# Performance work log

Hardware: AMD Instinct MI355X
Metric: run time of the kernel (lower is better)

Reference implementation:

```python
import jax, jax.numpy as jnp
import numpy as np

CUBE_SIZE = 24
N_NEURONS = CUBE_SIZE ** 3  # 13824
INPUT_DIM = 512
OUTPUT_DIM = 1000
MAX_STEPS = 30
BATCH = 256


def _build_neighbor_indices(size: int) -> np.ndarray:
    """[N, 27] int32; invalid (out-of-cube) neighbors map to pad slot N."""
    n = size ** 3
    c = np.arange(size)
    z, y, x = np.meshgrid(c, c, c, indexing='ij')  # each [size,size,size]
    cols = []
    for dz in (-1, 0, 1):
        for dy in (-1, 0, 1):
            for dx in (-1, 0, 1):
                nz, ny, nx = z + dz, y + dy, x + dx
                valid = ((nz >= 0) & (nz < size) & (ny >= 0) & (ny < size)
                         & (nx >= 0) & (nx < size))
                idx = nz * size * size + ny * size + nx
                cols.append(np.where(valid, idx, n))
    return np.stack(cols, axis=-1).reshape(n, 27).astype(np.int32)


def setup_inputs() -> dict:
    key = jax.random.key(0)
    ks = jax.random.split(key, 4)
    # xavier-ish small init scales (gain 0.5 style)
    w_in = jax.random.normal(ks[0], (N_NEURONS, INPUT_DIM), jnp.float32) * 0.01
    w_local = jax.random.normal(ks[1], (N_NEURONS, 27), jnp.float32) * 0.1
    w_out = jax.random.normal(ks[2], (OUTPUT_DIM, N_NEURONS), jnp.float32) * 0.01
    x = jax.random.normal(ks[3], (BATCH, INPUT_DIM), jnp.float32)
    return {
        'x': x,
        'W_in_w': w_in,
        'W_in_b': jnp.zeros((N_NEURONS,), jnp.float32),
        'W_local': w_local,
        'W_out_w': w_out,
        'W_out_b': jnp.zeros((OUTPUT_DIM,), jnp.float32),
        'neighbor_indices': jnp.asarray(_build_neighbor_indices(CUBE_SIZE)),
    }


def reference(x, W_in_w, W_in_b, W_local, W_out_w, W_out_b, neighbor_indices):
    batch = x.shape[0]
    x_proj = x @ W_in_w.T + W_in_b  # [B, N]
    h0 = jnp.zeros((batch, N_NEURONS), x.dtype)
    pad = jnp.zeros((batch, 1), x.dtype)

    def step(h, _):
        h_padded = jnp.concatenate([h, pad], axis=1)        # [B, N+1]
        nbr = h_padded[:, neighbor_indices]                  # [B, N, 27]
        weighted = jnp.einsum('bnk,nk->bn', nbr, W_local)    # [B, N]
        return jnp.tanh(x_proj + weighted), None

    h, _ = jax.lax.scan(step, h0, None, length=MAX_STEPS)
    return h @ W_out_w.T + W_out_b  # [B, output_dim]
```

## Files before the change

### kernel.cpp

```cpp
#include <hip/hip_runtime.h>
#include <hip/hip_bf16.h>

#define NN   13824
#define BB   256
#define KDIM 512
#define ODIM 1000
#define CUBE 24
#define KS   16

typedef short bf8 __attribute__((ext_vector_type(8)));
typedef float f32x4 __attribute__((ext_vector_type(4)));

__device__ __forceinline__ float fast_tanh(float a) {
    float e = __expf(2.0f * a);
    return 1.0f - 2.0f / (e + 1.0f);
}
__device__ __forceinline__ float bf_lo(unsigned u) { return __uint_as_float(u << 16); }
__device__ __forceinline__ float bf_hi(unsigned u) { return __uint_as_float(u & 0xffff0000u); }
__device__ __forceinline__ unsigned short bf_rne(float f) {
    unsigned u = __float_as_uint(f);
    u += 0x7fffu + ((u >> 16) & 1u);
    return (unsigned short)(u >> 16);
}
__device__ __forceinline__ unsigned pk_bf16(float lo, float hi) {
    union { __hip_bfloat162 h; unsigned u; } cv;
    cv.h = __float22bfloat162_rn(make_float2(lo, hi));
    return cv.u;
}
__device__ __forceinline__ bf8 cvt8(float4 a, float4 b) {
    union { bf8 v; unsigned u[4]; } r;
    r.u[0] = pk_bf16(a.x, a.y);
    r.u[1] = pk_bf16(a.z, a.w);
    r.u[2] = pk_bf16(b.x, b.y);
    r.u[3] = pk_bf16(b.z, b.w);
    return r.v;
}

__global__ __launch_bounds__(256) void xbf_kernel(
    const float* __restrict__ x, unsigned* __restrict__ xb)
{
    int i = blockIdx.x * 256 + threadIdx.x;
    float2 v = *(const float2*)&x[(size_t)i * 2];
    xb[i] = pk_bf16(v.x, v.y);
}

__global__ __launch_bounds__(256) void xproj_mfma(
    const float* __restrict__ w_in, const float* __restrict__ bias,
    const short* __restrict__ xbf, unsigned short* __restrict__ xp,
    unsigned short* __restrict__ h1)
{
    const int tid = threadIdx.x, w = tid >> 6, lane = tid & 63;
    const int quad = lane >> 4, l16 = lane & 15;
    const int n0 = blockIdx.x * 16;
    const float* __restrict__ arow = &w_in[(size_t)(n0 + l16) * KDIM];

    f32x4 acc[4] = {};

    int ka = quad * 8;
    float4 a0 = *(const float4*)&arow[ka];
    float4 a1 = *(const float4*)&arow[ka + 4];
    bf8 bb[4];
#pragma unroll
    for (int j = 0; j < 4; ++j)
        bb[j] = *(const bf8*)&xbf[(size_t)(w * 64 + j * 16 + l16) * KDIM + ka];

    for (int it = 0; it < 16; ++it) {
        float4 na0{}, na1{}; bf8 nb[4] = {};
        if (it < 15) {
            const int nka = ka + 32;
            na0 = *(const float4*)&arow[nka];
            na1 = *(const float4*)&arow[nka + 4];
#pragma unroll
            for (int j = 0; j < 4; ++j)
                nb[j] = *(const bf8*)&xbf[(size_t)(w * 64 + j * 16 + l16) * KDIM + nka];
        }
        bf8 af = cvt8(a0, a1);
#pragma unroll
        for (int j = 0; j < 4; ++j)
            acc[j] = __builtin_amdgcn_mfma_f32_16x16x32_bf16(af, bb[j], acc[j], 0, 0, 0);
        a0 = na0; a1 = na1;
#pragma unroll
        for (int j = 0; j < 4; ++j) bb[j] = nb[j];
        ka += 32;
    }

#pragma unroll
    for (int j = 0; j < 4; ++j) {
        const int b = w * 64 + j * 16 + l16;
#pragma unroll
        for (int r = 0; r < 4; ++r) {
            const int n = n0 + quad * 4 + r;
            const float v = acc[j][r] + bias[n];
            xp[(size_t)n * BB + b] = bf_rne(v);
            h1[(size_t)n * BB + b] = bf_rne(fast_tanh(v));
        }
    }
}

__device__ __forceinline__ void load_plane_f2(
    const unsigned* __restrict__ h32, int z, int y, int xx, int dof, float2* w9)
{
#pragma unroll
    for (int j = 0; j < 9; ++j) {
        const int dz = j / 3 - 1, dy = j % 3 - 1;
        const int zz = z + dz, yy = y + dy;
        const bool valid = (xx >= 0) & (xx < CUBE) & (zz >= 0) & (zz < CUBE) &
                           (yy >= 0) & (yy < CUBE);
        unsigned v = 0u;
        if (valid) v = h32[(size_t)((zz * 24 + yy) * 24 + xx) * 128 + dof];
        w9[j] = make_float2(bf_lo(v), bf_hi(v));
    }
}

__global__ __launch_bounds__(128) void step_kernel(
    const unsigned* __restrict__ hprev, const unsigned* __restrict__ xp,
    const float* __restrict__ wl, unsigned* __restrict__ hnext)
{
    const int tid  = threadIdx.x;
    const int wv   = __builtin_amdgcn_readfirstlane(tid >> 6);
    const int lane = tid & 63;

    const int bid   = blockIdx.x;
    const int zhi   = bid & 7;
    const int inner = bid >> 3;
    const int y     = inner % 24;
    const int r     = inner / 24;
    const int xc    = r & 3;
    const int zlo   = r >> 2;
    const int z     = zhi * 3 + zlo;

    const int x0   = xc * 6;
    const int dof  = wv * 64 + lane;

    float2 win[5][9];
    load_plane_f2(hprev, z, y, x0 - 1, dof, win[0]);
    load_plane_f2(hprev, z, y, x0,     dof, win[1]);
    load_plane_f2(hprev, z, y, x0 + 1, dof, win[2]);
    load_plane_f2(hprev, z, y, x0 + 2, dof, win[3]);

#pragma unroll
    for (int xi = 0; xi < 6; ++xi) {
        const int x = x0 + xi;
        if (xi <= 3)
            load_plane_f2(hprev, z, y, x + 3, dof, win[(xi + 4) % 5]);

        const int n = (z * 24 + y) * 24 + x;
        const float* __restrict__ wn = &wl[(size_t)n * 27];
        const unsigned xpv = xp[(size_t)n * 128 + dof];
        float2 acc = make_float2(bf_lo(xpv), bf_hi(xpv));

        const float2* pm = win[xi % 5];
        const float2* pc = win[(xi + 1) % 5];
        const float2* pp = win[(xi + 2) % 5];
#pragma unroll
        for (int j = 0; j < 9; ++j) {
            const float w0 = wn[3 * j + 0];
            const float w1 = wn[3 * j + 1];
            const float w2 = wn[3 * j + 2];
            acc.x += w0 * pm[j].x + w1 * pc[j].x + w2 * pp[j].x;
            acc.y += w0 * pm[j].y + w1 * pc[j].y + w2 * pp[j].y;
        }
        hnext[(size_t)n * 128 + dof] = pk_bf16(fast_tanh(acc.x), fast_tanh(acc.y));
    }
}

__global__ __launch_bounds__(256) void transpose_kernel(
    const unsigned* __restrict__ h32, unsigned* __restrict__ hT32)
{
    __shared__ unsigned short T[64][66];
    const int tid = threadIdx.x;
    const int rr = tid >> 2, g = tid & 3;
    const int k0 = blockIdx.x * 64, b0 = blockIdx.y * 64;
#pragma unroll
    for (int i = 0; i < 8; ++i) {
        unsigned d = h32[(size_t)(k0 + rr) * 128 + b0 / 2 + g * 8 + i];
        const int bl = (g * 8 + i) * 2;
        T[bl][rr]     = (unsigned short)(d & 0xffffu);
        T[bl + 1][rr] = (unsigned short)(d >> 16);
    }
    __syncthreads();
#pragma unroll
    for (int i = 0; i < 8; ++i) {
        const int kl = (g * 8 + i) * 2;
        unsigned d = (unsigned)T[rr][kl] | ((unsigned)T[rr][kl + 1] << 16);
        hT32[(size_t)(b0 + rr) * (NN / 2) + k0 / 2 + g * 8 + i] = d;
    }
}

__global__ __launch_bounds__(256) void outgemm_mfma(
    const float* __restrict__ wout, const short* __restrict__ hT,
    float* __restrict__ part)
{
    const int tid = threadIdx.x, w = tid >> 6, lane = tid & 63;
    const int quad = lane >> 4, l16 = lane & 15;
    const int o0 = blockIdx.x * 32;
    const int kb = blockIdx.y * (NN / KS);
    const int b0 = w * 64;

    const int oa = o0 + l16, ob = o0 + 16 + l16;
    const bool av0 = oa < ODIM, av1 = ob < ODIM;
    const float* __restrict__ ar0 = &wout[(size_t)oa * NN];
    const float* __restrict__ ar1 = &wout[(size_t)ob * NN];
    const float4 z4 = {0.f, 0.f, 0.f, 0.f};

    f32x4 acc[2][4] = {};

    int ka = kb + quad * 8;
    float4 a00 = av0 ? *(const float4*)&ar0[ka]     : z4;
    float4 a01 = av0 ? *(const float4*)&ar0[ka + 4] : z4;
    float4 a10 = av1 ? *(const float4*)&ar1[ka]     : z4;
    float4 a11 = av1 ? *(const float4*)&ar1[ka + 4] : z4;
    bf8 bb[4];
#pragma unroll
    for (int j = 0; j < 4; ++j)
        bb[j] = *(const bf8*)&hT[(size_t)(b0 + j * 16 + l16) * NN + ka];

    for (int it = 0; it < 27; ++it) {
        float4 na00{}, na01{}, na10{}, na11{}; bf8 nb[4] = {};
        if (it < 26) {
            const int nka = ka + 32;
            na00 = av0 ? *(const float4*)&ar0[nka]     : z4;
            na01 = av0 ? *(const float4*)&ar0[nka + 4] : z4;
            na10 = av1 ? *(const float4*)&ar1[nka]     : z4;
            na11 = av1 ? *(const float4*)&ar1[nka + 4] : z4;
#pragma unroll
            for (int j = 0; j < 4; ++j)
                nb[j] = *(const bf8*)&hT[(size_t)(b0 + j * 16 + l16) * NN + nka];
        }
        bf8 af0 = cvt8(a00, a01);
        bf8 af1 = cvt8(a10, a11);
#pragma unroll
        for (int j = 0; j < 4; ++j) {
            acc[0][j] = __builtin_amdgcn_mfma_f32_16x16x32_bf16(af0, bb[j], acc[0][j], 0, 0, 0);
            acc[1][j] = __builtin_amdgcn_mfma_f32_16x16x32_bf16(af1, bb[j], acc[1][j], 0, 0, 0);
        }
        a00 = na00; a01 = na01; a10 = na10; a11 = na11;
#pragma unroll
        for (int j = 0; j < 4; ++j) bb[j] = nb[j];
        ka += 32;
    }

#pragma unroll
    for (int i = 0; i < 2; ++i)
#pragma unroll
        for (int j = 0; j < 4; ++j) {
            const int b = b0 + j * 16 + l16;
#pragma unroll
            for (int r = 0; r < 4; ++r) {
                const int o = o0 + i * 16 + quad * 4 + r;
                part[((size_t)blockIdx.y * 1024 + o) * BB + b] = acc[i][j][r];
            }
        }
}

__global__ __launch_bounds__(256) void reduce_kernel(
    const float* __restrict__ part, const float* __restrict__ bias,
    float* __restrict__ out)
{
    const int o = blockIdx.x, b = threadIdx.x;
    float s = bias[o];
#pragma unroll
    for (int kc = 0; kc < KS; ++kc)
        s += part[((size_t)kc * 1024 + o) * BB + b];
    out[(size_t)b * ODIM + o] = s;
}

extern "C" void kernel_launch(void* const* d_in, const int* in_sizes, int n_in,
                              void* d_out, int out_size, void* d_ws, size_t ws_size,
                              hipStream_t stream)
{
    const float* x       = (const float*)d_in[0];
    const float* w_in    = (const float*)d_in[1];
    const float* b_in    = (const float*)d_in[2];
    const float* w_local = (const float*)d_in[3];
    const float* w_out   = (const float*)d_in[4];
    const float* b_out   = (const float*)d_in[5];
    float* out = (float*)d_out;

    char* p = (char*)d_ws;
    unsigned short* xp_bf = (unsigned short*)p;          p += (size_t)NN * BB * 2;
    unsigned short* hA    = (unsigned short*)p;          p += (size_t)NN * BB * 2;
    unsigned short* hB    = (unsigned short*)p;          p += (size_t)NN * BB * 2;
    unsigned short* hT    = (unsigned short*)p;          p += (size_t)NN * BB * 2;
    unsigned short* x_bf  = (unsigned short*)p;          p += (size_t)BB * KDIM * 2;
    float*          part  = (float*)p;

    xbf_kernel<<<256, 256, 0, stream>>>(x, (unsigned*)x_bf);
    xproj_mfma<<<864, 256, 0, stream>>>(w_in, b_in, (const short*)x_bf, xp_bf, hA);

    const unsigned* hp = (const unsigned*)hA;
    unsigned* hn = (unsigned*)hB;
    for (int s = 0; s < 29; ++s) {
        step_kernel<<<2304, 128, 0, stream>>>(hp, (const unsigned*)xp_bf, w_local, hn);
        unsigned* t = (unsigned*)hp; hp = hn; hn = t;
    }

    transpose_kernel<<<dim3(216, 4), 256, 0, stream>>>(hp, (unsigned*)hT);
    outgemm_mfma<<<dim3(32, KS), 256, 0, stream>>>(w_out, (const short*)hT, part);
    reduce_kernel<<<ODIM, 256, 0, stream>>>(part, b_out, out);
}
```

Before: 573.4 us.

## Run all recurrent steps in one LDS-resident cube kernel per batch pair

Replaces the 29 per-step launches with one persistent kernel. Each workgroup keeps a padded 26^3 fp16 cube for two batch columns in shared memory, double-buffered, and iterates every step with packed fp16 dot2 stencils, which removes the global-memory round trips and launch overhead between steps. The local weights are pre-packed to fp16 and the output GEMM switches to fp16 MFMA, with the split-K factor reduced. This relies on about 140KB of dynamic LDS per workgroup and uses only 128 workgroups, and fp16 lowers precision for the stencil weights and activations.

```diff
diff --git a/kernel.cpp b/kernel.cpp
--- a/kernel.cpp
+++ b/kernel.cpp
@@ -6,9 +6,18 @@
 #define KDIM 512
 #define ODIM 1000
 #define CUBE 24
-#define KS   16
+#define KS   12
+
+#define PC    26
+#define PLANE (PC*PC)
+#define PCUBE (PC*PC*PC)
+#define COLU  17576
+#define BUFU  35152
+#define LDSB  140608
 
 typedef short bf8 __attribute__((ext_vector_type(8)));
+typedef _Float16 h8 __attribute__((ext_vector_type(8)));
+typedef _Float16 h2 __attribute__((ext_vector_type(2)));
 typedef float f32x4 __attribute__((ext_vector_type(4)));
 
 __device__ __forceinline__ float fast_tanh(float a) {
@@ -29,10 +38,32 @@
 }
 __device__ __forceinline__ bf8 cvt8(float4 a, float4 b) {
     union { bf8 v; unsigned u[4]; } r;
-    r.u[0] = pk_bf16(a.x, a.y);
-    r.u[1] = pk_bf16(a.z, a.w);
-    r.u[2] = pk_bf16(b.x, b.y);
-    r.u[3] = pk_bf16(b.z, b.w);
+    r.u[0] = pk_bf16(a.x, a.y); r.u[1] = pk_bf16(a.z, a.w);
+    r.u[2] = pk_bf16(b.x, b.y); r.u[3] = pk_bf16(b.z, b.w);
+    return r.v;
+}
+__device__ __forceinline__ unsigned short f16b(float a) {
+    union { _Float16 h; unsigned short s; } c; c.h = (_Float16)a; return c.s;
+}
+__device__ __forceinline__ h2 u2h(unsigned u) {
+    union { unsigned u; h2 h; } c; c.u = u; return c.h;
+}
+__device__ __forceinline__ float f16lo(unsigned u) { return (float)u2h(u).x; }
+__device__ __forceinline__ float f16hi(unsigned u) { return (float)u2h(u).y; }
+#if __has_builtin(__builtin_amdgcn_fdot2)
+__device__ __forceinline__ float dot2(unsigned w, unsigned v, float acc) {
+    return __builtin_amdgcn_fdot2(u2h(w), u2h(v), acc, false);
+}
+#else
+__device__ __forceinline__ float dot2(unsigned w, unsigned v, float acc) {
+    h2 W = u2h(w), V = u2h(v);
+    return acc + (float)W.x * (float)V.x + (float)W.y * (float)V.y;
+}
+#endif
+__device__ __forceinline__ h8 cvt8f(float4 a, float4 b) {
+    union { h8 v; unsigned short s[8]; } r;
+    r.s[0] = f16b(a.x); r.s[1] = f16b(a.y); r.s[2] = f16b(a.z); r.s[3] = f16b(a.w);
+    r.s[4] = f16b(b.x); r.s[5] = f16b(b.y); r.s[6] = f16b(b.z); r.s[7] = f16b(b.w);
     return r.v;
 }
 
@@ -44,10 +75,25 @@
     xb[i] = pk_bf16(v.x, v.y);
 }
 
+__global__ __launch_bounds__(256) void wprep_kernel(
+    const float* __restrict__ wl, unsigned* __restrict__ wab,
+    unsigned short* __restrict__ wc)
+{
+    int n = blockIdx.x * 256 + threadIdx.x;
+#pragma unroll
+    for (int j = 0; j < 9; ++j) {
+        float w0 = wl[n * 27 + 3 * j + 0];
+        float w1 = wl[n * 27 + 3 * j + 1];
+        float w2 = wl[n * 27 + 3 * j + 2];
+        wab[j * NN + n] = (unsigned)f16b(w0) | ((unsigned)f16b(w1) << 16);
+        wc[j * NN + n]  = f16b(w2);
+    }
+}
+
 __global__ __launch_bounds__(256) void xproj_mfma(
     const float* __restrict__ w_in, const float* __restrict__ bias,
-    const short* __restrict__ xbf, unsigned short* __restrict__ xp,
-    unsigned short* __restrict__ h1)
+    const short* __restrict__ xbf, unsigned short* __restrict__ xpT_u,
+    unsigned short* __restrict__ xp_bf, unsigned short* __restrict__ h1)
 {
     const int tid = threadIdx.x, w = tid >> 6, lane = tid & 63;
     const int quad = lane >> 4, l16 = lane & 15;
@@ -91,9 +137,97 @@
         for (int r = 0; r < 4; ++r) {
             const int n = n0 + quad * 4 + r;
             const float v = acc[j][r] + bias[n];
-            xp[(size_t)n * BB + b] = bf_rne(v);
-            h1[(size_t)n * BB + b] = bf_rne(fast_tanh(v));
-        }
+            xp_bf[(size_t)n * BB + b] = bf_rne(v);
+            h1[(size_t)n * BB + b]    = bf_rne(fast_tanh(v));
+            xpT_u[((size_t)(b >> 1) * NN + n) * 2 + (b & 1)] = f16b(v);
+        }
+    }
+}
+
+__global__ __launch_bounds__(512) void cube_kernel(
+    const unsigned* __restrict__ xpT,
+    const unsigned* __restrict__ wab,
+    const unsigned short* __restrict__ wc,
+    unsigned short* __restrict__ hT)
+{
+    extern __shared__ char smem[];
+    unsigned*        sdw = (unsigned*)smem;
+    unsigned short*  sus = (unsigned short*)smem;
+    const int tid = threadIdx.x;
+    const int cp  = blockIdx.x;
+
+    for (int i = tid; i < (LDSB / 4); i += 512) sdw[i] = 0u;
+    __syncthreads();
+
+#pragma unroll 1
+    for (int k = 0; k < 14; ++k) {
+        int p = tid + k * 512;
+        if (p >= 6912) break;
+        int line = p / 12, xq = p - line * 12, x0 = 2 * xq;
+        int z = line / 24, y = line - z * 24;
+        int n0 = line * 24 + x0;
+        uint2 xq2 = *(const uint2*)&xpT[(size_t)cp * NN + n0];
+        int Pi = ((z + 1) * PC + (y + 1)) * PC + x0 + 1;
+        sus[Pi]            = f16b(fast_tanh(f16lo(xq2.x)));
+        sus[Pi + 1]        = f16b(fast_tanh(f16lo(xq2.y)));
+        sus[COLU + Pi]     = f16b(fast_tanh(f16hi(xq2.x)));
+        sus[COLU + Pi + 1] = f16b(fast_tanh(f16hi(xq2.y)));
+    }
+    __syncthreads();
+
+    int cur = 0;
+#pragma unroll 1
+    for (int s = 0; s < 29; ++s) {
+        const int curU = cur * BUFU;
+        const int nxtU = curU ^ BUFU;
+#pragma unroll 1
+        for (int k = 0; k < 14; ++k) {
+            int p = tid + k * 512;
+            if (p >= 6912) break;
+            int line = p / 12, xq = p - line * 12, x0 = 2 * xq;
+            int z = line / 24, y = line - z * 24;
+            int n0 = line * 24 + x0;
+            int pb = curU + (z * PC + y) * PC + x0;
+
+            uint2 xq2 = *(const uint2*)&xpT[(size_t)cp * NN + n0];
+            float a00 = f16lo(xq2.x), a01 = f16hi(xq2.x);
+            float a10 = f16lo(xq2.y), a11 = f16hi(xq2.y);
+#pragma unroll
+            for (int j = 0; j < 9; ++j) {
+                const int off = (j / 3) * PLANE + (j % 3) * PC;
+                unsigned d0c0 = *(const unsigned*)&sus[pb + off];
+                unsigned d1c0 = *(const unsigned*)&sus[pb + off + 2];
+                unsigned d0c1 = *(const unsigned*)&sus[pb + off + COLU];
+                unsigned d1c1 = *(const unsigned*)&sus[pb + off + COLU + 2];
+                uint2 w2v = *(const uint2*)&wab[(size_t)j * NN + n0];
+                unsigned wcd = *(const unsigned*)&wc[(size_t)j * NN + n0];
+                unsigned wB0 = wcd & 0xffffu;
+                unsigned wB1 = wcd >> 16;
+                a00 = dot2(w2v.x, d0c0, a00); a00 = dot2(wB0, d1c0, a00);
+                a01 = dot2(w2v.x, d0c1, a01); a01 = dot2(wB0, d1c1, a01);
+                unsigned s1c0 = __builtin_amdgcn_alignbit(d1c0, d0c0, 16);
+                unsigned s3c0 = d1c0 >> 16;
+                unsigned s1c1 = __builtin_amdgcn_alignbit(d1c1, d0c1, 16);
+                unsigned s3c1 = d1c1 >> 16;
+                a10 = dot2(w2v.y, s1c0, a10); a10 = dot2(wB1, s3c0, a10);
+                a11 = dot2(w2v.y, s1c1, a11); a11 = dot2(wB1, s3c1, a11);
+            }
+            int Pw = nxtU + (pb - curU) + PLANE + PC + 1;
+            sus[Pw]            = f16b(fast_tanh(a00));
+            sus[Pw + 1]        = f16b(fast_tanh(a10));
+            sus[Pw + COLU]     = f16b(fast_tanh(a01));
+            sus[Pw + COLU + 1] = f16b(fast_tanh(a11));
+        }
+        __syncthreads();
+        cur ^= 1;
+    }
+
+    const int fU = cur * BUFU;
+    for (int n = tid; n < NN; n += 512) {
+        int z = n / 576, r = n - z * 576, y = r / 24, x = r - y * 24;
+        int P = fU + ((z + 1) * PC + (y + 1)) * PC + x + 1;
+        hT[(size_t)(2 * cp) * NN + n]     = sus[P];
+        hT[(size_t)(2 * cp + 1) * NN + n] = sus[P + COLU];
     }
 }
 
@@ -119,7 +253,6 @@
     const int tid  = threadIdx.x;
     const int wv   = __builtin_amdgcn_readfirstlane(tid >> 6);
     const int lane = tid & 63;
-
     const int bid   = blockIdx.x;
     const int zhi   = bid & 7;
     const int inner = bid >> 3;
@@ -128,9 +261,8 @@
     const int xc    = r & 3;
     const int zlo   = r >> 2;
     const int z     = zhi * 3 + zlo;
-
-    const int x0   = xc * 6;
-    const int dof  = wv * 64 + lane;
+    const int x0    = xc * 6;
+    const int dof   = wv * 64 + lane;
 
     float2 win[5][9];
     load_plane_f2(hprev, z, y, x0 - 1, dof, win[0]);
@@ -141,22 +273,17 @@
 #pragma unroll
     for (int xi = 0; xi < 6; ++xi) {
         const int x = x0 + xi;
-        if (xi <= 3)
-            load_plane_f2(hprev, z, y, x + 3, dof, win[(xi + 4) % 5]);
-
+        if (xi <= 3) load_plane_f2(hprev, z, y, x + 3, dof, win[(xi + 4) % 5]);
         const int n = (z * 24 + y) * 24 + x;
         const float* __restrict__ wn = &wl[(size_t)n * 27];
         const unsigned xpv = xp[(size_t)n * 128 + dof];
         float2 acc = make_float2(bf_lo(xpv), bf_hi(xpv));
-
         const float2* pm = win[xi % 5];
         const float2* pc = win[(xi + 1) % 5];
         const float2* pp = win[(xi + 2) % 5];
 #pragma unroll
         for (int j = 0; j < 9; ++j) {
-            const float w0 = wn[3 * j + 0];
-            const float w1 = wn[3 * j + 1];
-            const float w2 = wn[3 * j + 2];
+            const float w0 = wn[3 * j], w1 = wn[3 * j + 1], w2 = wn[3 * j + 2];
             acc.x += w0 * pm[j].x + w1 * pc[j].x + w2 * pp[j].x;
             acc.y += w0 * pm[j].y + w1 * pc[j].y + w2 * pp[j].y;
         }
@@ -164,7 +291,7 @@
     }
 }
 
-__global__ __launch_bounds__(256) void transpose_kernel(
+__global__ __launch_bounds__(256) void transpose_cvt(
     const unsigned* __restrict__ h32, unsigned* __restrict__ hT32)
 {
     __shared__ unsigned short T[64][66];
@@ -182,13 +309,15 @@
 #pragma unroll
     for (int i = 0; i < 8; ++i) {
         const int kl = (g * 8 + i) * 2;
-        unsigned d = (unsigned)T[rr][kl] | ((unsigned)T[rr][kl + 1] << 16);
-        hT32[(size_t)(b0 + rr) * (NN / 2) + k0 / 2 + g * 8 + i] = d;
+        float fa = __uint_as_float((unsigned)T[rr][kl] << 16);
+        float fb = __uint_as_float((unsigned)T[rr][kl + 1] << 16);
+        hT32[(size_t)(b0 + rr) * (NN / 2) + k0 / 2 + g * 8 + i] =
+            (unsigned)f16b(fa) | ((unsigned)f16b(fb) << 16);
     }
 }
 
 __global__ __launch_bounds__(256) void outgemm_mfma(
-    const float* __restrict__ wout, const short* __restrict__ hT,
+    const float* __restrict__ wout, const _Float16* __restrict__ hT,
     float* __restrict__ part)
 {
     const int tid = threadIdx.x, w = tid >> 6, lane = tid & 63;
@@ -210,14 +339,15 @@
     float4 a01 = av0 ? *(const float4*)&ar0[ka + 4] : z4;
     float4 a10 = av1 ? *(const float4*)&ar1[ka]     : z4;
     float4 a11 = av1 ? *(const float4*)&ar1[ka + 4] : z4;
-    bf8 bb[4];
+    h8 bb[4];
 #pragma unroll
     for (int j = 0; j < 4; ++j)
-        bb[j] = *(const bf8*)&hT[(size_t)(b0 + j * 16 + l16) * NN + ka];
-
-    for (int it = 0; it < 27; ++it) {
-        float4 na00{}, na01{}, na10{}, na11{}; bf8 nb[4] = {};
-        if (it < 26) {
+        bb[j] = *(const h8*)&hT[(size_t)(b0 + j * 16 + l16) * NN + ka];
+
+    const int ITER = (NN / KS) / 32;
+    for (int it = 0; it < ITER; ++it) {
+        float4 na00{}, na01{}, na10{}, na11{}; h8 nb[4] = {};
+        if (it < ITER - 1) {
             const int nka = ka + 32;
             na00 = av0 ? *(const float4*)&ar0[nka]     : z4;
             na01 = av0 ? *(const float4*)&ar0[nka + 4] : z4;
@@ -225,14 +355,14 @@
             na11 = av1 ? *(const float4*)&ar1[nka + 4] : z4;
 #pragma unroll
             for (int j = 0; j < 4; ++j)
-                nb[j] = *(const bf8*)&hT[(size_t)(b0 + j * 16 + l16) * NN + nka];
-        }
-        bf8 af0 = cvt8(a00, a01);
-        bf8 af1 = cvt8(a10, a11);
+                nb[j] = *(const h8*)&hT[(size_t)(b0 + j * 16 + l16) * NN + nka];
+        }
+        h8 af0 = cvt8f(a00, a01);
+        h8 af1 = cvt8f(a10, a11);
 #pragma unroll
         for (int j = 0; j < 4; ++j) {
-            acc[0][j] = __builtin_amdgcn_mfma_f32_16x16x32_bf16(af0, bb[j], acc[0][j], 0, 0, 0);
-            acc[1][j] = __builtin_amdgcn_mfma_f32_16x16x32_bf16(af1, bb[j], acc[1][j], 0, 0, 0);
+            acc[0][j] = __builtin_amdgcn_mfma_f32_16x16x32_f16(af0, bb[j], acc[0][j], 0, 0, 0);
+            acc[1][j] = __builtin_amdgcn_mfma_f32_16x16x32_f16(af1, bb[j], acc[1][j], 0, 0, 0);
         }
         a00 = na00; a01 = na01; a10 = na10; a11 = na11;
 #pragma unroll
@@ -278,24 +408,36 @@
     float* out = (float*)d_out;
 
     char* p = (char*)d_ws;
-    unsigned short* xp_bf = (unsigned short*)p;          p += (size_t)NN * BB * 2;
-    unsigned short* hA    = (unsigned short*)p;          p += (size_t)NN * BB * 2;
-    unsigned short* hB    = (unsigned short*)p;          p += (size_t)NN * BB * 2;
-    unsigned short* hT    = (unsigned short*)p;          p += (size_t)NN * BB * 2;
-    unsigned short* x_bf  = (unsigned short*)p;          p += (size_t)BB * KDIM * 2;
-    float*          part  = (float*)p;
+    unsigned*       xpT   = (unsigned*)p;        p += (size_t)128 * NN * 4;
+    unsigned short* hT    = (unsigned short*)p;  p += (size_t)256 * NN * 2;
+    unsigned short* x_bf  = (unsigned short*)p;  p += (size_t)BB * KDIM * 2;
+    unsigned*       wab   = (unsigned*)p;        p += (size_t)9 * NN * 4;
+    unsigned short* wc    = (unsigned short*)p;  p += (size_t)9 * NN * 2;
+    unsigned short* xp_bf = (unsigned short*)p;  p += (size_t)NN * BB * 2;
+    unsigned short* hA    = (unsigned short*)p;  p += (size_t)NN * BB * 2;
+    unsigned short* hB    = (unsigned short*)p;  p += (size_t)NN * BB * 2;
+    float* part = (float*)xp_bf;
 
     xbf_kernel<<<256, 256, 0, stream>>>(x, (unsigned*)x_bf);
-    xproj_mfma<<<864, 256, 0, stream>>>(w_in, b_in, (const short*)x_bf, xp_bf, hA);
-
-    const unsigned* hp = (const unsigned*)hA;
-    unsigned* hn = (unsigned*)hB;
-    for (int s = 0; s < 29; ++s) {
-        step_kernel<<<2304, 128, 0, stream>>>(hp, (const unsigned*)xp_bf, w_local, hn);
-        unsigned* t = (unsigned*)hp; hp = hn; hn = t;
-    }
-
-    transpose_kernel<<<dim3(216, 4), 256, 0, stream>>>(hp, (unsigned*)hT);
-    outgemm_mfma<<<dim3(32, KS), 256, 0, stream>>>(w_out, (const short*)hT, part);
+    wprep_kernel<<<54, 256, 0, stream>>>(w_local, wab, wc);
+    xproj_mfma<<<864, 256, 0, stream>>>(w_in, b_in, (const short*)x_bf,
+                                        (unsigned short*)xpT, xp_bf, hA);
+
+    bool fast = hipFuncSetAttribute((const void*)cube_kernel,
+        hipFuncAttributeMaxDynamicSharedMemorySize, LDSB) == hipSuccess;
+
+    if (fast) {
+        cube_kernel<<<128, 512, LDSB, stream>>>(xpT, wab, wc, hT);
+    } else {
+        const unsigned* hp = (const unsigned*)hA;
+        unsigned* hn = (unsigned*)hB;
+        for (int s = 0; s < 29; ++s) {
+            step_kernel<<<2304, 128, 0, stream>>>(hp, (const unsigned*)xp_bf, w_local, hn);
+            unsigned* t = (unsigned*)hp; hp = hn; hn = t;
+        }
+        transpose_cvt<<<dim3(216, 4), 256, 0, stream>>>((const unsigned*)hB, (unsigned*)hT);
+    }
+
+    outgemm_mfma<<<dim3(32, KS), 256, 0, stream>>>(w_out, (const _Float16*)hT, part);
     reduce_kernel<<<ODIM, 256, 0, stream>>>(part, b_out, out);
 }
```

Result: slower. 922.6 us (+60.9%).
